# Performance work log

Hardware: AMD Instinct MI355X
Metric: run time of the kernel (lower is better)

The kernel has to match this reference:

```python
import jax, jax.numpy as jnp
import numpy as np

GROUP_SIZE = 64
QMAX = 7.0   # int4 symmetric: clamp(round(x/s), -8, 7), zero-point = 0
QMIN = -8.0
EPS = 1e-8


def _group_quant_dequant(t, group_size):
    """Symmetric per-group int4 quantize + dequantize along the last dim.

    t: [..., F] with F % group_size == 0
    Returns dequantized tensor of same shape (equals q_int * scale, which is
    mathematically what the packed int4 GEMM with inline scale dequant computes).
    """
    shp = t.shape
    tg = t.reshape(shp[:-1] + (shp[-1] // group_size, group_size))
    scale = jnp.max(jnp.abs(tg), axis=-1, keepdims=True) / QMAX
    scale = jnp.maximum(scale, EPS)
    q = jnp.clip(jnp.round(tg / scale), QMIN, QMAX)
    return (q * scale).reshape(shp)


def setup_inputs() -> dict:
    key = jax.random.key(0)
    k1, k2 = jax.random.split(key)
    x = jax.random.normal(k1, (8192, 4096), dtype=jnp.float32)
    weight = jax.random.normal(k2, (4096, 4096), dtype=jnp.float32) * 0.02
    return {"x": x, "weight": weight}


def reference(x, weight):
    # ActQuantizerGS: per-token, per-group-of-64 symmetric int4 quant of x.
    x_dq = _group_quant_dequant(x, GROUP_SIZE)          # [T, K]
    # WeightQuantizer + LinearFLHGS: per-(out_channel, group) symmetric int4
    # weight quant; GEMM with inline scale dequant. Because scales are constant
    # within each group, int-accumulate-then-scale == dequant-then-matmul.
    w_dq = _group_quant_dequant(weight, GROUP_SIZE)     # [O, K]
    return x_dq @ w_dq.T                                # [T, O]
```

## Files before the change

kernel.cpp:

```cpp
#include <hip/hip_runtime.h>
#include <hip/hip_bf16.h>
#include <stdint.h>


typedef __bf16 bf16x8 __attribute__((ext_vector_type(8)));
typedef float f32x4 __attribute__((ext_vector_type(4)));

static __device__ __forceinline__ uint16_t f32_to_bf16_rne(float f) {
    uint32_t u = __float_as_uint(f);
    uint32_t r = (u + 0x7fffu + ((u >> 16) & 1u)) >> 16;
    return (uint16_t)r;
}

__global__ void quant_kernel(const float* __restrict__ in,
                             uint16_t* __restrict__ out, int total4) {
    int nthreads = gridDim.x * blockDim.x;
    int t = blockIdx.x * blockDim.x + threadIdx.x;
    for (int i = t; i < total4; i += nthreads) {
        float4 v = ((const float4*)in)[i];
        float amax = fmaxf(fmaxf(fabsf(v.x), fabsf(v.y)),
                           fmaxf(fabsf(v.z), fabsf(v.w)));
        #pragma unroll
        for (int m = 1; m <= 8; m <<= 1)
            amax = fmaxf(amax, __shfl_xor(amax, m, 64));
        float s = fmaxf(amax / 7.0f, 1e-8f);
        float q0 = fminf(fmaxf(rintf(v.x / s), -8.0f), 7.0f);
        float q1 = fminf(fmaxf(rintf(v.y / s), -8.0f), 7.0f);
        float q2 = fminf(fmaxf(rintf(v.z / s), -8.0f), 7.0f);
        float q3 = fminf(fmaxf(rintf(v.w / s), -8.0f), 7.0f);
        ushort4 o;
        o.x = f32_to_bf16_rne(q0 * s);
        o.y = f32_to_bf16_rne(q1 * s);
        o.z = f32_to_bf16_rne(q2 * s);
        o.w = f32_to_bf16_rne(q3 * s);
        ((ushort4*)out)[i] = o;
    }
}

#define BM 256
#define BN 256
#define BK 64

#define FENCE() asm volatile("" ::: "memory")
#define SB0()   __builtin_amdgcn_sched_barrier(0)

__global__ __launch_bounds__(512, 2) void gemm_kernel(
        const uint16_t* __restrict__ A, const uint16_t* __restrict__ B,
        float* __restrict__ C, int M, int N, int K) {
    __shared__ uint16_t As[2][2][128 * 64];
    __shared__ uint16_t Bs[2][2][128 * 64];

    const int NTt = K >> 6;

    int nwg = gridDim.x;
    int bid = blockIdx.x;
    int swz = bid;
    if ((nwg & 7) == 0) {
        int cpx = nwg >> 3;
        swz = (bid & 7) * cpx + (bid >> 3);
    }
    int nbn = N / BN;
    int bm = swz / nbn, bn = swz % nbn;

    int tid = threadIdx.x;
    int lane = tid & 63;
    int wid = tid >> 6;
    int wm = wid >> 2;
    int wn = wid & 3;

    const int rowA0 = bm * BM;
    const int colB0 = bn * BN;

    int srow = lane >> 3;
    int scol = ((lane & 7) ^ (lane >> 3)) << 3;

    int rl = lane & 15;
    int cg = lane >> 4;
    int coff[2];
    coff[0] = ((0 + cg) ^ (rl & 7)) << 3;
    coff[1] = ((4 + cg) ^ (rl & 7)) << 3;

    const int bhalf = wn >> 1;
    const int brow0 = (wn & 1) * 64;

    f32x4 acc[8][4] = {};
    bf16x8 A0[4][2], A1[4][2], B0[2][2], B1[2][2];

    auto stageA = [&](int buf, int half, int t) {
        #pragma unroll
        for (int j = 0; j < 2; ++j) {
            int rowin = wid * 16 + j * 8;
            const uint16_t* g = A + (size_t)(rowA0 + half * 128 + rowin + srow) * K
                                  + t * 64 + scol;
            uint16_t* l = &As[buf][half][rowin * 64];
            __builtin_amdgcn_global_load_lds(
                (const __attribute__((address_space(1))) void*)g,
                (__attribute__((address_space(3))) void*)l, 16, 0, 0);
        }
    };
    auto stageB = [&](int buf, int half, int t) {
        #pragma unroll
        for (int j = 0; j < 2; ++j) {
            int rowin = wid * 16 + j * 8;
            const uint16_t* g = B + (size_t)(colB0 + half * 128 + rowin + srow) * K
                                  + t * 64 + scol;
            uint16_t* l = &Bs[buf][half][rowin * 64];
            __builtin_amdgcn_global_load_lds(
                (const __attribute__((address_space(1))) void*)g,
                (__attribute__((address_space(3))) void*)l, 16, 0, 0);
        }
    };

    auto readA4 = [&](bf16x8 (&dst)[4][2], int lo, int buf) {
        #pragma unroll
        for (int mi = 0; mi < 4; ++mi)
            #pragma unroll
            for (int ks = 0; ks < 2; ++ks)
                dst[mi][ks] =
                    *(const bf16x8*)&As[buf][wm][((lo + mi) * 16 + rl) * 64 + coff[ks]];
    };
    auto readB2 = [&](bf16x8 (&dst)[2][2], int lo, int buf) {
        #pragma unroll
        for (int ni = 0; ni < 2; ++ni)
            #pragma unroll
            for (int ks = 0; ks < 2; ++ks)
                dst[ni][ks] =
                    *(const bf16x8*)&Bs[buf][bhalf][(brow0 + (lo + ni) * 16 + rl) * 64 + coff[ks]];
    };

    auto quad = [&](const bf16x8 (&af)[4][2], const bf16x8 (&bf)[2][2],
                    int mo, int no) {
        __builtin_amdgcn_s_setprio(1);
        #pragma unroll
        for (int mi = 0; mi < 4; ++mi)
            #pragma unroll
            for (int ni = 0; ni < 2; ++ni)
                #pragma unroll
                for (int ks = 0; ks < 2; ++ks)
                    acc[mo + mi][no + ni] = __builtin_amdgcn_mfma_f32_16x16x32_bf16(
                        af[mi][ks], bf[ni][ks], acc[mo + mi][no + ni], 0, 0, 0);
        __builtin_amdgcn_s_setprio(0);
    };

    stageA(0, 0, 0); stageA(0, 1, 0); stageB(0, 0, 0); stageB(0, 1, 0);
    stageA(1, 0, 1); stageA(1, 1, 1); stageB(1, 0, 1); stageB(1, 1, 1);
    asm volatile("s_waitcnt vmcnt(8)" ::: "memory");
    FENCE(); __builtin_amdgcn_s_barrier(); FENCE();
    readA4(A0, 0, 0);
    readB2(B0, 0, 0);

    for (int t = 0; t < NTt; ++t) {
        int ct = t & 1, nt = ct ^ 1;

        readA4(A1, 4, ct);
        readB2(B1, 2, ct);
        SB0();
        quad(A0, B0, 0, 0);
        SB0();

        asm volatile("s_waitcnt lgkmcnt(0)" ::: "memory");
        SB0();
        FENCE(); __builtin_amdgcn_s_barrier(); FENCE();
        if (t + 2 < NTt) {
            stageA(ct, 0, t + 2); stageA(ct, 1, t + 2);
            stageB(ct, 0, t + 2); stageB(ct, 1, t + 2);
        }
        SB0();

        quad(A1, B0, 4, 0);
        SB0();

        if (t + 2 < NTt) asm volatile("s_waitcnt vmcnt(8)" ::: "memory");
        else             asm volatile("s_waitcnt vmcnt(0)" ::: "memory");
        FENCE(); __builtin_amdgcn_s_barrier(); FENCE();

        if (t + 1 < NTt) readB2(B0, 0, nt);
        SB0();
        quad(A0, B1, 0, 2);
        SB0();

        if (t + 1 < NTt) readA4(A0, 0, nt);
        SB0();
        quad(A1, B1, 4, 2);
        SB0();
    }

    int cl = lane & 15;
    int rq = (lane >> 4) * 4;
    #pragma unroll
    for (int mi = 0; mi < 8; ++mi) {
        #pragma unroll
        for (int ni = 0; ni < 4; ++ni) {
            int row = rowA0 + wm * 128 + mi * 16 + rq;
            int col = colB0 + wn * 64 + ni * 16 + cl;
            float* cp = C + (size_t)row * N + col;
            #pragma unroll
            for (int r = 0; r < 4; ++r)
                cp[(size_t)r * N] = acc[mi][ni][r];
        }
    }
}

extern "C" void kernel_launch(void* const* d_in, const int* in_sizes, int n_in,
                              void* d_out, int out_size, void* d_ws, size_t ws_size,
                              hipStream_t stream) {
    const float* x = (const float*)d_in[0];
    const float* w = (const float*)d_in[1];
    float* out = (float*)d_out;

    const int K = 4096;
    const int T = in_sizes[0] / K;
    const int O = in_sizes[1] / K;

    uint16_t* xq = (uint16_t*)d_ws;
    uint16_t* wq = (uint16_t*)((char*)d_ws + (size_t)T * K * 2);

    quant_kernel<<<2048, 256, 0, stream>>>(x, xq, (T * K) >> 2);
    quant_kernel<<<2048, 256, 0, stream>>>(w, wq, (O * K) >> 2);

    int nwg = (T / BM) * (O / BN);
    gemm_kernel<<<nwg, 512, 0, stream>>>(xq, wq, out, T, O, K);
}
```

Baseline: 328.1 us.

## Restructure GEMM main loop into 8-phase ping-pong schedule with interleaved staging

Replaces the per-K-tile loop with an unrolled two-tile iteration split into eight phases, each bracketed by barriers and priority raises around a quarter of the MFMA work. Global-to-LDS staging of the next tiles is spread across phases, and the wait counts are retuned to match. The aim is finer overlap between LDS reads, global loads and MFMA issue across the two co-resident waves. The cost is more barriers per tile, and the partial-wait accounting could race if the counts are wrong.

```diff
diff --git a/kernel.cpp b/kernel.cpp
--- a/kernel.cpp
+++ b/kernel.cpp
@@ -44,6 +44,16 @@
 #define FENCE() asm volatile("" ::: "memory")
 #define SB0()   __builtin_amdgcn_sched_barrier(0)
 
+#define PH_MID() \
+    FENCE(); __builtin_amdgcn_s_barrier(); \
+    asm volatile("s_waitcnt lgkmcnt(0)" ::: "memory"); \
+    SB0(); \
+    __builtin_amdgcn_s_setprio(1);
+
+#define PH_END() \
+    __builtin_amdgcn_s_setprio(0); \
+    FENCE(); __builtin_amdgcn_s_barrier(); FENCE();
+
 __global__ __launch_bounds__(512, 2) void gemm_kernel(
         const uint16_t* __restrict__ A, const uint16_t* __restrict__ B,
         float* __restrict__ C, int M, int N, int K) {
@@ -51,6 +61,7 @@
     __shared__ uint16_t Bs[2][2][128 * 64];
 
     const int NTt = K >> 6;
+    const int NIter = NTt >> 1;
 
     int nwg = gridDim.x;
     int bid = blockIdx.x;
@@ -84,7 +95,7 @@
     const int brow0 = (wn & 1) * 64;
 
     f32x4 acc[8][4] = {};
-    bf16x8 A0[4][2], A1[4][2], B0[2][2], B1[2][2];
+    bf16x8 aLo[4][2], aHi[4][2], bLo[2][2], bHi[2][2];
 
     auto stageA = [&](int buf, int half, int t) {
         #pragma unroll
@@ -111,26 +122,23 @@
         }
     };
 
-    auto readA4 = [&](bf16x8 (&dst)[4][2], int lo, int buf) {
+    auto readA = [&](bf16x8 (&dst)[4][2], int lo, int buf) {
         #pragma unroll
         for (int mi = 0; mi < 4; ++mi)
             #pragma unroll
             for (int ks = 0; ks < 2; ++ks)
-                dst[mi][ks] =
-                    *(const bf16x8*)&As[buf][wm][((lo + mi) * 16 + rl) * 64 + coff[ks]];
-    };
-    auto readB2 = [&](bf16x8 (&dst)[2][2], int lo, int buf) {
+                dst[mi][ks] = *(const bf16x8*)&As[buf][wm][((lo + mi) * 16 + rl) * 64 + coff[ks]];
+    };
+    auto readB = [&](bf16x8 (&dst)[2][2], int lo, int buf) {
         #pragma unroll
         for (int ni = 0; ni < 2; ++ni)
             #pragma unroll
             for (int ks = 0; ks < 2; ++ks)
-                dst[ni][ks] =
-                    *(const bf16x8*)&Bs[buf][bhalf][(brow0 + (lo + ni) * 16 + rl) * 64 + coff[ks]];
-    };
-
-    auto quad = [&](const bf16x8 (&af)[4][2], const bf16x8 (&bf)[2][2],
-                    int mo, int no) {
-        __builtin_amdgcn_s_setprio(1);
+                dst[ni][ks] = *(const bf16x8*)&Bs[buf][bhalf][(brow0 + (lo + ni) * 16 + rl) * 64 + coff[ks]];
+    };
+
+    auto quadQ = [&](const bf16x8 (&af)[4][2], const bf16x8 (&bf)[2][2],
+                     int mo, int no) {
         #pragma unroll
         for (int mi = 0; mi < 4; ++mi)
             #pragma unroll
@@ -139,50 +147,51 @@
                 for (int ks = 0; ks < 2; ++ks)
                     acc[mo + mi][no + ni] = __builtin_amdgcn_mfma_f32_16x16x32_bf16(
                         af[mi][ks], bf[ni][ks], acc[mo + mi][no + ni], 0, 0, 0);
-        __builtin_amdgcn_s_setprio(0);
     };
 
     stageA(0, 0, 0); stageA(0, 1, 0); stageB(0, 0, 0); stageB(0, 1, 0);
-    stageA(1, 0, 1); stageA(1, 1, 1); stageB(1, 0, 1); stageB(1, 1, 1);
-    asm volatile("s_waitcnt vmcnt(8)" ::: "memory");
+    stageB(1, 0, 1); stageB(1, 1, 1); stageA(1, 0, 1);
+    asm volatile("s_waitcnt vmcnt(6)" ::: "memory");
     FENCE(); __builtin_amdgcn_s_barrier(); FENCE();
-    readA4(A0, 0, 0);
-    readB2(B0, 0, 0);
-
-    for (int t = 0; t < NTt; ++t) {
-        int ct = t & 1, nt = ct ^ 1;
-
-        readA4(A1, 4, ct);
-        readB2(B1, 2, ct);
-        SB0();
-        quad(A0, B0, 0, 0);
-        SB0();
-
-        asm volatile("s_waitcnt lgkmcnt(0)" ::: "memory");
-        SB0();
-        FENCE(); __builtin_amdgcn_s_barrier(); FENCE();
-        if (t + 2 < NTt) {
-            stageA(ct, 0, t + 2); stageA(ct, 1, t + 2);
-            stageB(ct, 0, t + 2); stageB(ct, 1, t + 2);
-        }
-        SB0();
-
-        quad(A1, B0, 4, 0);
-        SB0();
-
-        if (t + 2 < NTt) asm volatile("s_waitcnt vmcnt(8)" ::: "memory");
-        else             asm volatile("s_waitcnt vmcnt(0)" ::: "memory");
-        FENCE(); __builtin_amdgcn_s_barrier(); FENCE();
-
-        if (t + 1 < NTt) readB2(B0, 0, nt);
-        SB0();
-        quad(A0, B1, 0, 2);
-        SB0();
-
-        if (t + 1 < NTt) readA4(A0, 0, nt);
-        SB0();
-        quad(A1, B1, 4, 2);
-        SB0();
+
+    for (int i = 0; i < NIter; ++i) {
+        int u = 2 * i, v = u + 1;
+        const bool g2 = (u + 2 < NTt), g3 = (u + 3 < NTt);
+        const bool last = (i == NIter - 1);
+
+        readA(aLo, 0, 0); readB(bLo, 0, 0);
+        stageA(1, 1, v);
+        asm volatile("s_waitcnt lgkmcnt(8)" ::: "memory");
+        PH_MID(); quadQ(aLo, bLo, 0, 0); PH_END();
+
+        readB(bHi, 2, 0);
+        PH_MID(); quadQ(aLo, bHi, 0, 2); PH_END();
+
+        readA(aHi, 4, 0);
+        if (g2) stageB(0, 0, u + 2);
+        PH_MID(); quadQ(aHi, bLo, 4, 0); PH_END();
+
+        if (g2) { stageB(0, 1, u + 2); stageA(0, 0, u + 2); }
+        if (last) asm volatile("s_waitcnt vmcnt(0)" ::: "memory");
+        else      asm volatile("s_waitcnt vmcnt(6)" ::: "memory");
+        PH_MID(); quadQ(aHi, bHi, 4, 2); PH_END();
+
+        readA(aLo, 0, 1); readB(bLo, 0, 1);
+        if (g2) stageA(0, 1, u + 2);
+        asm volatile("s_waitcnt lgkmcnt(8)" ::: "memory");
+        PH_MID(); quadQ(aLo, bLo, 0, 0); PH_END();
+
+        readB(bHi, 2, 1);
+        PH_MID(); quadQ(aLo, bHi, 0, 2); PH_END();
+
+        readA(aHi, 4, 1);
+        if (g3) stageB(1, 0, u + 3);
+        PH_MID(); quadQ(aHi, bLo, 4, 0); PH_END();
+
+        if (g3) { stageB(1, 1, u + 3); stageA(1, 0, u + 3); }
+        if (last) asm volatile("s_waitcnt vmcnt(0)" ::: "memory");
+        else      asm volatile("s_waitcnt vmcnt(6)" ::: "memory");
+        PH_MID(); quadQ(aHi, bHi, 4, 2); PH_END();
     }
 
     int cl = lane & 15;
```

New measurement: 320.3 us. 2.4% less time.

## Restructure GEMM main loop into barrier-interleaved four-phase MFMA schedule

Applied to the files above, without the earlier changes.

Reorders the per-iteration schedule of the bf16 GEMM into four phases, each issuing LDS fragment reads, a workgroup barrier, a partial lgkmcnt wait and one MFMA quadrant at raised priority. Global-to-LDS staging for tile t+2 moves to the last phase, and a full vmcnt(0) wait now happens once per iteration. The aim is lockstep ping-pong between waves so LDS reads and MFMA work overlap across waves. In exchange it adds many more barriers per iteration and gives global prefetch less slack, which could stall the pipeline.

```diff
diff --git a/kernel.cpp b/kernel.cpp
--- a/kernel.cpp
+++ b/kernel.cpp
@@ -84,7 +84,7 @@
     const int brow0 = (wn & 1) * 64;
 
     f32x4 acc[8][4] = {};
-    bf16x8 A0[4][2], A1[4][2], B0[2][2], B1[2][2];
+    bf16x8 aLo[4][2], aHi[4][2], bLo[2][2], bHi[2][2];
 
     auto stageA = [&](int buf, int half, int t) {
         #pragma unroll
@@ -111,26 +111,23 @@
         }
     };
 
-    auto readA4 = [&](bf16x8 (&dst)[4][2], int lo, int buf) {
+    auto readA = [&](bf16x8 (&dst)[4][2], int lo, int buf) {
         #pragma unroll
         for (int mi = 0; mi < 4; ++mi)
             #pragma unroll
             for (int ks = 0; ks < 2; ++ks)
-                dst[mi][ks] =
-                    *(const bf16x8*)&As[buf][wm][((lo + mi) * 16 + rl) * 64 + coff[ks]];
-    };
-    auto readB2 = [&](bf16x8 (&dst)[2][2], int lo, int buf) {
+                dst[mi][ks] = *(const bf16x8*)&As[buf][wm][((lo + mi) * 16 + rl) * 64 + coff[ks]];
+    };
+    auto readB = [&](bf16x8 (&dst)[2][2], int lo, int buf) {
         #pragma unroll
         for (int ni = 0; ni < 2; ++ni)
             #pragma unroll
             for (int ks = 0; ks < 2; ++ks)
-                dst[ni][ks] =
-                    *(const bf16x8*)&Bs[buf][bhalf][(brow0 + (lo + ni) * 16 + rl) * 64 + coff[ks]];
-    };
-
-    auto quad = [&](const bf16x8 (&af)[4][2], const bf16x8 (&bf)[2][2],
-                    int mo, int no) {
-        __builtin_amdgcn_s_setprio(1);
+                dst[ni][ks] = *(const bf16x8*)&Bs[buf][bhalf][(brow0 + (lo + ni) * 16 + rl) * 64 + coff[ks]];
+    };
+
+    auto quadQ = [&](const bf16x8 (&af)[4][2], const bf16x8 (&bf)[2][2],
+                     int mo, int no) {
         #pragma unroll
         for (int mi = 0; mi < 4; ++mi)
             #pragma unroll
@@ -139,50 +136,52 @@
                 for (int ks = 0; ks < 2; ++ks)
                     acc[mo + mi][no + ni] = __builtin_amdgcn_mfma_f32_16x16x32_bf16(
                         af[mi][ks], bf[ni][ks], acc[mo + mi][no + ni], 0, 0, 0);
-        __builtin_amdgcn_s_setprio(0);
     };
 
     stageA(0, 0, 0); stageA(0, 1, 0); stageB(0, 0, 0); stageB(0, 1, 0);
     stageA(1, 0, 1); stageA(1, 1, 1); stageB(1, 0, 1); stageB(1, 1, 1);
     asm volatile("s_waitcnt vmcnt(8)" ::: "memory");
     FENCE(); __builtin_amdgcn_s_barrier(); FENCE();
-    readA4(A0, 0, 0);
-    readB2(B0, 0, 0);
+    readA(aLo, 0, 0); readB(bLo, 0, 0);
 
     for (int t = 0; t < NTt; ++t) {
-        int ct = t & 1, nt = ct ^ 1;
-
-        readA4(A1, 4, ct);
-        readB2(B1, 2, ct);
-        SB0();
-        quad(A0, B0, 0, 0);
-        SB0();
-
+        int cb = t & 1, nb = cb ^ 1;
+
+        readB(bHi, 2, cb);
+        FENCE(); __builtin_amdgcn_s_barrier();
+        asm volatile("s_waitcnt lgkmcnt(4)" ::: "memory");
+        SB0(); __builtin_amdgcn_s_setprio(1);
+        quadQ(aLo, bLo, 0, 0);
+        __builtin_amdgcn_s_setprio(0);
+        FENCE(); __builtin_amdgcn_s_barrier(); FENCE();
+
+        readA(aHi, 4, cb);
+        FENCE(); __builtin_amdgcn_s_barrier();
+        asm volatile("s_waitcnt lgkmcnt(8)" ::: "memory");
+        SB0(); __builtin_amdgcn_s_setprio(1);
+        quadQ(aLo, bHi, 0, 2);
+        __builtin_amdgcn_s_setprio(0);
+        FENCE(); __builtin_amdgcn_s_barrier(); FENCE();
+
+        asm volatile("s_waitcnt vmcnt(0)" ::: "memory");
+        FENCE(); __builtin_amdgcn_s_barrier();
         asm volatile("s_waitcnt lgkmcnt(0)" ::: "memory");
-        SB0();
-        FENCE(); __builtin_amdgcn_s_barrier(); FENCE();
+        SB0(); __builtin_amdgcn_s_setprio(1);
+        quadQ(aHi, bLo, 4, 0);
+        __builtin_amdgcn_s_setprio(0);
+        if (t + 1 < NTt) readB(bLo, 0, nb);
+        FENCE(); __builtin_amdgcn_s_barrier(); FENCE();
+
         if (t + 2 < NTt) {
-            stageA(ct, 0, t + 2); stageA(ct, 1, t + 2);
-            stageB(ct, 0, t + 2); stageB(ct, 1, t + 2);
-        }
-        SB0();
-
-        quad(A1, B0, 4, 0);
-        SB0();
-
-        if (t + 2 < NTt) asm volatile("s_waitcnt vmcnt(8)" ::: "memory");
-        else             asm volatile("s_waitcnt vmcnt(0)" ::: "memory");
-        FENCE(); __builtin_amdgcn_s_barrier(); FENCE();
-
-        if (t + 1 < NTt) readB2(B0, 0, nt);
-        SB0();
-        quad(A0, B1, 0, 2);
-        SB0();
-
-        if (t + 1 < NTt) readA4(A0, 0, nt);
-        SB0();
-        quad(A1, B1, 4, 2);
-        SB0();
+            stageA(cb, 0, t + 2); stageA(cb, 1, t + 2);
+            stageB(cb, 0, t + 2); stageB(cb, 1, t + 2);
+        }
+        if (t + 1 < NTt) readA(aLo, 0, nb);
+        FENCE(); __builtin_amdgcn_s_barrier();
+        SB0(); __builtin_amdgcn_s_setprio(1);
+        quadQ(aHi, bHi, 4, 2);
+        __builtin_amdgcn_s_setprio(0);
+        FENCE(); __builtin_amdgcn_s_barrier(); FENCE();
     }
 
     int cl = lane & 15;
```

After: 378.4 us. +15.3%, slower.
